# Kernel tuning notes

Hardware: AMD Instinct MI355X
Metric: run time of the kernel (lower is better)

Reference implementation:

```python
import jax, jax.numpy as jnp
import numpy as np

HEADS = 16
NUM_CHUNKS = 8  # min(int(log2(4096))+1, 8)


def setup_inputs() -> dict:
    key = jax.random.key(0)
    ks = jax.random.split(key, 6)
    B, T, C = 4, 4096, 1024
    s = 1.0 / np.sqrt(C)
    x = jax.random.normal(ks[0], (B, T, C), jnp.float32)
    Wqkv = jax.random.normal(ks[1], (3 * C, C), jnp.float32) * s
    Wout = jax.random.normal(ks[2], (C, C), jnp.float32) * s
    bout = jnp.zeros((C,), jnp.float32)
    Wl1 = jax.random.normal(ks[3], (64, 1), jnp.float32)
    bl1 = jnp.zeros((64,), jnp.float32)
    Wl2 = jax.random.normal(ks[4], (HEADS, 64), jnp.float32) * 0.125
    bl2 = jnp.zeros((HEADS,), jnp.float32)
    return dict(x=x, Wqkv=Wqkv, Wout=Wout, bout=bout, Wl1=Wl1, bl1=bl1, Wl2=Wl2, bl2=bl2)


def reference(x, Wqkv, Wout, bout, Wl1, bl1, Wl2, bl2):
    B, T, C = x.shape
    H = HEADS
    dh = C // H
    nc = NUM_CHUNKS
    cs = T // nc
    scale = dh ** (-0.5)

    # qkv projection (torch Linear: x @ W.T), split, to [B,H,T,dh]
    qkv = x @ Wqkv.T  # [B,T,3C]
    q, k, v = jnp.split(qkv, 3, axis=-1)
    def heads(t):
        return t.reshape(B, T, H, dh).transpose(0, 2, 1, 3)
    q, k, v = heads(q), heads(k), heads(v)

    # lambda gates from log positions: [T,1] -> [T,H] -> [H,T]
    log_pos = jnp.log(jnp.arange(T, dtype=jnp.float32) + 1.0)[:, None]
    h1 = jax.nn.relu(log_pos @ Wl1.T + bl1)            # [T,64]
    lam = jax.nn.sigmoid(h1 @ Wl2.T + bl2).T           # [H,T]
    lam = lam.reshape(H, nc, cs)                        # per-chunk key gates

    # block-local (chunked) attention, fully vectorized over chunks
    qc = q.reshape(B, H, nc, cs, dh)
    kc = k.reshape(B, H, nc, cs, dh)
    vc = v.reshape(B, H, nc, cs, dh)
    scores = jnp.einsum('bhnqd,bhnkd->bhnqk', qc, kc) * scale
    scores = scores * lam[None, :, :, None, :]          # gate keys pre-softmax
    attn = jax.nn.softmax(scores, axis=-1)
    out = jnp.einsum('bhnqk,bhnkd->bhnqd', attn, vc)    # [B,H,nc,cs,dh]

    out = out.reshape(B, H, T, dh).transpose(0, 2, 1, 3).reshape(B, T, C)
    return out @ Wout.T + bout
```

## Files before the change

### kernel.cpp

```cpp
#include <hip/hip_runtime.h>
#include <hip/hip_bf16.h>

typedef unsigned short u16;
typedef __attribute__((ext_vector_type(8))) short v8s;
typedef __attribute__((ext_vector_type(4))) float v4f;
typedef __attribute__((ext_vector_type(4))) unsigned v4u;

#define DEV __device__ __forceinline__

DEV u16 f2bf(float f) {
  union { float f; unsigned u; } v; v.f = f;
  unsigned r = v.u + 0x7fffu + ((v.u >> 16) & 1u);
  return (u16)(r >> 16);
}

DEV unsigned pk2bf(float a, float b) {
  float2 t; t.x = a; t.y = b;
  __hip_bfloat162 p = __float22bfloat162_rn(t);
  union { __hip_bfloat162 h; unsigned u; } c; c.h = p;
  return c.u;
}

DEV void gload_lds16(const void* g, void* l) {
  __builtin_amdgcn_global_load_lds(
      (const __attribute__((address_space(1))) void*)g,
      (__attribute__((address_space(3))) void*)l, 16, 0, 0);
}

__global__ __launch_bounds__(256) void cvt_bf16(const float* __restrict__ in,
                                                u16* __restrict__ out, int n4) {
  int i = blockIdx.x * 256 + threadIdx.x;
  if (i >= n4) return;
  float4 v = ((const float4*)in)[i];
  ushort4 o;
  o.x = f2bf(v.x); o.y = f2bf(v.y); o.z = f2bf(v.z); o.w = f2bf(v.w);
  ((ushort4*)out)[i] = o;
}

__global__ __launch_bounds__(256) void lam_kernel(const float* __restrict__ Wl1,
    const float* __restrict__ bl1, const float* __restrict__ Wl2,
    const float* __restrict__ bl2, float* __restrict__ lam) {
  int t = blockIdx.x * 256 + threadIdx.x;
  float lp = logf((float)t + 1.0f);
  float h1[64];
#pragma unroll
  for (int j = 0; j < 64; ++j) h1[j] = fmaxf(lp * Wl1[j] + bl1[j], 0.0f);
#pragma unroll 1
  for (int h = 0; h < 16; ++h) {
    float z = bl2[h];
#pragma unroll
    for (int j = 0; j < 64; ++j) z += h1[j] * Wl2[h * 64 + j];
    lam[h * 4096 + t] = 0.125f / (1.0f + expf(-z));
  }
}

template <int MH, int NH>
DEV void mfma16(v4f (&acc)[8][4], const v8s (&a)[4][2], const v8s (&b)[2][2]) {
#pragma unroll
  for (int kk = 0; kk < 2; ++kk)
#pragma unroll
    for (int i = 0; i < 4; ++i)
#pragma unroll
      for (int j = 0; j < 2; ++j)
        acc[MH * 4 + i][NH * 2 + j] = __builtin_amdgcn_mfma_f32_16x16x32_bf16(
            a[i][kk], b[j][kk], acc[MH * 4 + i][NH * 2 + j], 0, 0, 0);
}

DEV void ldA(v8s (&a)[4][2], const u16* Ab, int wr, int mh, int lane) {
  const int l15 = lane & 15, g = lane >> 4;
#pragma unroll
  for (int i = 0; i < 4; ++i) {
    const int row = wr * 128 + mh * 64 + i * 16 + l15;
#pragma unroll
    for (int kk = 0; kk < 2; ++kk)
      a[i][kk] = *(const v8s*)(Ab + row * 64 + (((kk * 4 + g) ^ (row & 7)) << 3));
  }
}

DEV void ldB(v8s (&b)[2][2], const u16* Bb, int wc, int nh, int lane) {
  const int l15 = lane & 15, g = lane >> 4;
#pragma unroll
  for (int j = 0; j < 2; ++j) {
    const int row = nh * 128 + wc * 32 + j * 16 + l15;
#pragma unroll
    for (int kk = 0; kk < 2; ++kk)
      b[j][kk] = *(const v8s*)(Bb + row * 64 + (((kk * 4 + g) ^ (row & 7)) << 3));
  }
}

template <int OUTF32>
__global__ __launch_bounds__(512, 2) void gemm256(const u16* __restrict__ A,
    const u16* __restrict__ Bt, void* __restrict__ Cout,
    const float* __restrict__ bias, int M, int N, int K) {
  __shared__ u16 As[2][256 * 64];
  __shared__ u16 Bs[2][256 * 64];
  const int tid = threadIdx.x;
  const int lane = tid & 63;
  const int nbn = N >> 8;
  const int nwg = gridDim.x;
  int wg = blockIdx.x;
  wg = (wg & 7) * (nwg >> 3) + (wg >> 3);
  const int m0 = (wg / nbn) << 8;
  const int n0 = (wg % nbn) << 8;
  const int wid = tid >> 6;
  const int wr = wid >> 2;
  const int wc = wid & 3;
  const int nkt = K >> 6;
  const int nit = nkt >> 1;

  auto SAu = [&](int buf, int kt, int u) {
    const int ur = tid >> 3;
    const int slot = (tid & 7) ^ (ur & 7);
    gload_lds16(A + (size_t)(m0 + u * 64 + ur) * K + kt * 64 + slot * 8,
                &As[buf][u * 4096 + (tid & ~63) * 8]);
  };
  auto SBu = [&](int buf, int kt, int u) {
    const int q = tid >> 3;
    const int grow = (((u & 1) * 2 + (q >> 5)) << 6) + ((u >> 1) << 5) + (q & 31);
    const int slot = (tid & 7) ^ (q & 7);
    gload_lds16(Bt + (size_t)(n0 + grow) * K + kt * 64 + slot * 8,
                &Bs[buf][u * 4096 + (tid & ~63) * 8]);
  };
  auto SA_ = [&](int buf, int kt, int mh) { SAu(buf, kt, mh); SAu(buf, kt, 2 + mh); };
  auto SB_ = [&](int buf, int kt, int nh) { SBu(buf, kt, nh * 2); SBu(buf, kt, nh * 2 + 1); };

  v4f acc[8][4] = {};
  v8s a[4][2], b[2][2];

  SA_(0, 0, 0); SB_(0, 0, 0); SB_(0, 0, 1); SA_(0, 0, 1);
  SA_(1, 1 < nkt ? 1 : 0, 0); SB_(1, 1 < nkt ? 1 : 0, 1); SA_(1, 1 < nkt ? 1 : 0, 1);
  asm volatile("s_waitcnt vmcnt(6)" ::: "memory");
  asm volatile("s_barrier" ::: "memory");

#define PHASE(MHc, NHc, STAGE, VM)                      \
  STAGE;                                                \
  asm volatile("s_barrier" ::: "memory");               \
  __builtin_amdgcn_sched_barrier(0);                    \
  __builtin_amdgcn_s_setprio(1);                        \
  mfma16<MHc, NHc>(acc, a, b);                          \
  __builtin_amdgcn_s_setprio(0);                        \
  if (VM) asm volatile("s_waitcnt vmcnt(6)" ::: "memory"); \
  asm volatile("s_barrier" ::: "memory");

  for (int it = 0; it < nit; ++it) {
    const int t0 = 2 * it;
    const int tn = t0 + 1;
    const int ta = (t0 + 2 < nkt) ? t0 + 2 : nkt - 1;
    const int tb = (t0 + 3 < nkt) ? t0 + 3 : nkt - 1;
    ldA(a, As[0], wr, 0, lane); ldB(b, Bs[0], wc, 0, lane);
    PHASE(0, 0, SB_(1, tn, 0), 0);
    ldB(b, Bs[0], wc, 1, lane);
    PHASE(0, 1, SA_(0, ta, 0), 0);
    ldA(a, As[0], wr, 1, lane);
    PHASE(1, 1, SB_(0, ta, 1), 0);
    ldB(b, Bs[0], wc, 0, lane);
    PHASE(1, 0, SA_(0, ta, 1), 1);
    ldA(a, As[1], wr, 0, lane); ldB(b, Bs[1], wc, 0, lane);
    PHASE(0, 0, SB_(0, ta, 0), 0);
    ldB(b, Bs[1], wc, 1, lane);
    PHASE(0, 1, SA_(1, tb, 0), 0);
    ldA(a, As[1], wr, 1, lane);
    PHASE(1, 1, SB_(1, tb, 1), 0);
    ldB(b, Bs[1], wc, 0, lane);
    PHASE(1, 0, SA_(1, tb, 1), 1);
  }
#undef PHASE

  const int l15 = lane & 15, g4 = (lane >> 4) * 4;
#pragma unroll
  for (int i = 0; i < 8; ++i) {
#pragma unroll
    for (int j = 0; j < 4; ++j) {
      const int gr = m0 + wr * 128 + i * 16 + g4;
      const int gc = n0 + wc * 64 + j * 16 + l15;
      float bv = OUTF32 ? bias[gc] : 0.0f;
#pragma unroll
      for (int r = 0; r < 4; ++r) {
        float val = acc[i][j][r];
        if (OUTF32) ((float*)Cout)[(size_t)(gr + r) * N + gc] = val + bv;
        else ((u16*)Cout)[(size_t)(gr + r) * N + gc] = f2bf(val);
      }
    }
  }
}

__global__ __launch_bounds__(512, 2) void attn_chunk(const u16* __restrict__ qkv,
    const float* __restrict__ lam, u16* __restrict__ aout) {
  __shared__ u16 Ksm[512 * 64];
  __shared__ u16 Vt[64 * 520];
  __shared__ float lam_s[512];

  const int tid = threadIdx.x;
  const int lane = tid & 63;
  const int wid = tid >> 6;
  const int blk = blockIdx.x;
  const int c = blk & 7;
  const int h = (blk >> 3) & 15;
  const int b = blk >> 7;
  const size_t tok0 = (size_t)b * 4096 + c * 512;
  const u16* qb = qkv + tok0 * 3072 + h * 64;
  const u16* kb = qb + 1024;
  const u16* vb = qb + 2048;

  lam_s[tid] = lam[h * 4096 + c * 512 + tid];

#pragma unroll
  for (int i = 0; i < 8; ++i) {
    const int r = i * 64 + wid * 8 + (lane >> 3);
    const int f = (r & 3) | (((r >> 3) & 1) << 2);
    gload_lds16(kb + (size_t)r * 3072 + (((lane & 7) ^ f) << 3),
                &Ksm[(i * 64 + wid * 8) * 64]);
  }
  {
    const int pr = tid & 255;
    const int db0 = (tid >> 8) * 4;
#pragma unroll
    for (int dbi = 0; dbi < 4; ++dbi) {
      const int d0 = (db0 + dbi) * 8;
      v8s v0 = *(const v8s*)(vb + (size_t)(2 * pr) * 3072 + d0);
      v8s v1 = *(const v8s*)(vb + (size_t)(2 * pr + 1) * 3072 + d0);
#pragma unroll
      for (int j = 0; j < 8; ++j) {
        unsigned pk = (unsigned)(u16)v0[j] | ((unsigned)(u16)v1[j] << 16);
        *(unsigned*)&Vt[(d0 + j) * 520 + 2 * pr] = pk;
      }
    }
  }
  __syncthreads();

  const int l15 = lane & 15;
  const int gg = lane >> 4;
  const int rbase = ((l15 >> 2) << 3) + (l15 & 3);
  const int fsl = (l15 & 3) | (((l15 >> 2) & 1) << 2);
  const int sl0 = ((gg ^ fsl) << 3);
  const int sl1 = (((4 + gg) ^ fsl) << 3);

#pragma unroll 1
  for (int pass = 0; pass < 4; ++pass) {
    const int q0 = pass * 128 + wid * 16;
    const v8s qf0 = *(const v8s*)(qb + (size_t)(q0 + l15) * 3072 + gg * 8);
    const v8s qf1 = *(const v8s*)(qb + (size_t)(q0 + l15) * 3072 + 32 + gg * 8);

    float m = -1e30f, sum = 0.0f;
    v4f o[4] = {};

#pragma unroll 1
    for (int qtr = 0; qtr < 4; ++qtr) {
      v4f s[8];
#pragma unroll
      for (int kpl = 0; kpl < 4; ++kpl) {
#pragma unroll
        for (int hh = 0; hh < 2; ++hh) {
          const int rw = (qtr * 128 + kpl * 32 + rbase + hh * 4) << 6;
          v4f z = {0.f, 0.f, 0.f, 0.f};
          z = __builtin_amdgcn_mfma_f32_16x16x32_bf16(
              *(const v8s*)&Ksm[rw + sl0], qf0, z, 0, 0, 0);
          z = __builtin_amdgcn_mfma_f32_16x16x32_bf16(
              *(const v8s*)&Ksm[rw + sl1], qf1, z, 0, 0, 0);
          const v4f lv = *(const v4f*)&lam_s[qtr * 128 + kpl * 32 + gg * 8 + hh * 4];
          s[kpl * 2 + hh] = z * lv;
        }
      }
      v4f vm = s[0];
#pragma unroll
      for (int kt = 1; kt < 8; ++kt)
#pragma unroll
        for (int r = 0; r < 4; ++r) vm[r] = fmaxf(vm[r], s[kt][r]);
      float qmax = fmaxf(fmaxf(vm[0], vm[1]), fmaxf(vm[2], vm[3]));
      qmax = fmaxf(qmax, __shfl_xor(qmax, 16));
      qmax = fmaxf(qmax, __shfl_xor(qmax, 32));
      const float newm = fmaxf(m, qmax);
      const float scale = __expf(m - newm);
      m = newm;
      float psum = 0.f;
#pragma unroll
      for (int kt = 0; kt < 8; ++kt)
#pragma unroll
        for (int r = 0; r < 4; ++r) {
          s[kt][r] = __expf(s[kt][r] - m);
          psum += s[kt][r];
        }
      sum = sum * scale + psum;
#pragma unroll
      for (int dt = 0; dt < 4; ++dt)
#pragma unroll
        for (int r = 0; r < 4; ++r) o[dt][r] *= scale;

#pragma unroll
      for (int kpl = 0; kpl < 4; ++kpl) {
        v4u pwv;
        pwv.x = pk2bf(s[2 * kpl][0], s[2 * kpl][1]);
        pwv.y = pk2bf(s[2 * kpl][2], s[2 * kpl][3]);
        pwv.z = pk2bf(s[2 * kpl + 1][0], s[2 * kpl + 1][1]);
        pwv.w = pk2bf(s[2 * kpl + 1][2], s[2 * kpl + 1][3]);
        const v8s pf = __builtin_bit_cast(v8s, pwv);
#pragma unroll
        for (int dt = 0; dt < 4; ++dt) {
          const v8s vf = *(const v8s*)&Vt[(dt * 16 + l15) * 520 +
                                          (qtr * 4 + kpl) * 32 + gg * 8];
          o[dt] = __builtin_amdgcn_mfma_f32_16x16x32_bf16(vf, pf, o[dt], 0, 0, 0);
        }
      }
    }

    sum += __shfl_xor(sum, 16);
    sum += __shfl_xor(sum, 32);
    const float sminv = 1.0f / sum;

    const size_t obase = (tok0 + q0 + l15) * 1024 + h * 64;
#pragma unroll
    for (int dt = 0; dt < 4; ++dt) {
      ushort4 w;
      w.x = f2bf(o[dt][0] * sminv); w.y = f2bf(o[dt][1] * sminv);
      w.z = f2bf(o[dt][2] * sminv); w.w = f2bf(o[dt][3] * sminv);
      *(ushort4*)&aout[obase + dt * 16 + gg * 4] = w;
    }
  }
}

extern "C" void kernel_launch(void* const* d_in, const int* in_sizes, int n_in,
                              void* d_out, int out_size, void* d_ws, size_t ws_size,
                              hipStream_t stream) {
  const float* x    = (const float*)d_in[0];
  const float* Wqkv = (const float*)d_in[1];
  const float* Wout = (const float*)d_in[2];
  const float* bout = (const float*)d_in[3];
  const float* Wl1  = (const float*)d_in[4];
  const float* bl1  = (const float*)d_in[5];
  const float* Wl2  = (const float*)d_in[6];
  const float* bl2  = (const float*)d_in[7];
  float* out = (float*)d_out;

  char* ws = (char*)d_ws;
  u16* xbf    = (u16*)ws; ws += (size_t)16384 * 1024 * 2;
  u16* wqkvbf = (u16*)ws; ws += (size_t)3072 * 1024 * 2;
  u16* woutbf = (u16*)ws; ws += (size_t)1024 * 1024 * 2;
  u16* qkvbf  = (u16*)ws; ws += (size_t)16384 * 3072 * 2;
  u16* aoutbf = (u16*)ws; ws += (size_t)16384 * 1024 * 2;
  float* lam  = (float*)ws; ws += (size_t)16 * 4096 * 4;

  cvt_bf16<<<16384, 256, 0, stream>>>(x, xbf, 16777216 / 4);
  cvt_bf16<<<3072, 256, 0, stream>>>(Wqkv, wqkvbf, 3145728 / 4);
  cvt_bf16<<<1024, 256, 0, stream>>>(Wout, woutbf, 1048576 / 4);
  lam_kernel<<<16, 256, 0, stream>>>(Wl1, bl1, Wl2, bl2, lam);

  gemm256<0><<<dim3((16384 / 256) * (3072 / 256)), 512, 0, stream>>>(
      xbf, wqkvbf, qkvbf, nullptr, 16384, 3072, 1024);

  attn_chunk<<<512, 512, 0, stream>>>(qkvbf, lam, aoutbf);

  gemm256<1><<<dim3((16384 / 256) * (1024 / 256)), 512, 0, stream>>>(
      aoutbf, woutbf, out, bout, 16384, 1024, 1024);
}
```

Baseline: 278.0 us.

## Restructure GEMM main loop into four wider MFMA phases with full B fragment

Each warp now loads the whole B fragment (4x2) at once and runs 32 MFMAs per phase instead of 16. That halves the barrier-separated phases per K-iteration from eight to four. The global-to-LDS staging schedule is reorganized to match. This reduces barrier and LDS-read overhead per MFMA, at the cost of more registers for B fragments and a different, riskier prefetch/waitcnt ordering.

```diff
diff --git a/kernel.cpp b/kernel.cpp
--- a/kernel.cpp
+++ b/kernel.cpp
@@ -54,16 +54,16 @@
   }
 }
 
-template <int MH, int NH>
-DEV void mfma16(v4f (&acc)[8][4], const v8s (&a)[4][2], const v8s (&b)[2][2]) {
+template <int MH>
+DEV void mfma32(v4f (&acc)[8][4], const v8s (&a)[4][2], const v8s (&b)[4][2]) {
 #pragma unroll
   for (int kk = 0; kk < 2; ++kk)
 #pragma unroll
     for (int i = 0; i < 4; ++i)
 #pragma unroll
-      for (int j = 0; j < 2; ++j)
-        acc[MH * 4 + i][NH * 2 + j] = __builtin_amdgcn_mfma_f32_16x16x32_bf16(
-            a[i][kk], b[j][kk], acc[MH * 4 + i][NH * 2 + j], 0, 0, 0);
+      for (int j = 0; j < 4; ++j)
+        acc[MH * 4 + i][j] = __builtin_amdgcn_mfma_f32_16x16x32_bf16(
+            a[i][kk], b[j][kk], acc[MH * 4 + i][j], 0, 0, 0);
 }
 
 DEV void ldA(v8s (&a)[4][2], const u16* Ab, int wr, int mh, int lane) {
@@ -77,11 +77,11 @@
   }
 }
 
-DEV void ldB(v8s (&b)[2][2], const u16* Bb, int wc, int nh, int lane) {
+DEV void ldB4(v8s (&b)[4][2], const u16* Bb, int wc, int lane) {
   const int l15 = lane & 15, g = lane >> 4;
 #pragma unroll
-  for (int j = 0; j < 2; ++j) {
-    const int row = nh * 128 + wc * 32 + j * 16 + l15;
+  for (int j = 0; j < 4; ++j) {
+    const int row = (j >> 1) * 128 + wc * 32 + (j & 1) * 16 + l15;
 #pragma unroll
     for (int kk = 0; kk < 2; ++kk)
       b[j][kk] = *(const v8s*)(Bb + row * 64 + (((kk * 4 + g) ^ (row & 7)) << 3));
@@ -125,44 +125,36 @@
   auto SB_ = [&](int buf, int kt, int nh) { SBu(buf, kt, nh * 2); SBu(buf, kt, nh * 2 + 1); };
 
   v4f acc[8][4] = {};
-  v8s a[4][2], b[2][2];
-
-  SA_(0, 0, 0); SB_(0, 0, 0); SB_(0, 0, 1); SA_(0, 0, 1);
-  SA_(1, 1 < nkt ? 1 : 0, 0); SB_(1, 1 < nkt ? 1 : 0, 1); SA_(1, 1 < nkt ? 1 : 0, 1);
+  v8s a[4][2], b[4][2];
+
+  SA_(0, 0, 0); SA_(0, 0, 1); SB_(0, 0, 0); SB_(0, 0, 1);
+  SA_(1, 1, 0); SB_(1, 1, 0); SB_(1, 1, 1);
   asm volatile("s_waitcnt vmcnt(6)" ::: "memory");
   asm volatile("s_barrier" ::: "memory");
 
-#define PHASE(MHc, NHc, STAGE, VM)                      \
-  STAGE;                                                \
-  asm volatile("s_barrier" ::: "memory");               \
-  __builtin_amdgcn_sched_barrier(0);                    \
-  __builtin_amdgcn_s_setprio(1);                        \
-  mfma16<MHc, NHc>(acc, a, b);                          \
-  __builtin_amdgcn_s_setprio(0);                        \
-  if (VM) asm volatile("s_waitcnt vmcnt(6)" ::: "memory"); \
+#define PHASE(MHc, VM, ...)                                 \
+  do { __VA_ARGS__; } while (0);                            \
+  asm volatile("s_barrier" ::: "memory");                   \
+  __builtin_amdgcn_sched_barrier(0);                        \
+  __builtin_amdgcn_s_setprio(1);                            \
+  mfma32<MHc>(acc, a, b);                                   \
+  __builtin_amdgcn_s_setprio(0);                            \
+  if (VM) asm volatile("s_waitcnt vmcnt(6)" ::: "memory");  \
   asm volatile("s_barrier" ::: "memory");
 
   for (int it = 0; it < nit; ++it) {
     const int t0 = 2 * it;
-    const int tn = t0 + 1;
-    const int ta = (t0 + 2 < nkt) ? t0 + 2 : nkt - 1;
-    const int tb = (t0 + 3 < nkt) ? t0 + 3 : nkt - 1;
-    ldA(a, As[0], wr, 0, lane); ldB(b, Bs[0], wc, 0, lane);
-    PHASE(0, 0, SB_(1, tn, 0), 0);
-    ldB(b, Bs[0], wc, 1, lane);
-    PHASE(0, 1, SA_(0, ta, 0), 0);
+    const int t1 = t0 + 1;
+    const int t2 = (t0 + 2 < nkt) ? t0 + 2 : nkt - 1;
+    const int t3 = (t0 + 3 < nkt) ? t0 + 3 : nkt - 1;
+    ldA(a, As[0], wr, 0, lane); ldB4(b, Bs[0], wc, lane);
+    PHASE(0, 0, SAu(1, t1, 1); SAu(1, t1, 3));
     ldA(a, As[0], wr, 1, lane);
-    PHASE(1, 1, SB_(0, ta, 1), 0);
-    ldB(b, Bs[0], wc, 0, lane);
-    PHASE(1, 0, SA_(0, ta, 1), 1);
-    ldA(a, As[1], wr, 0, lane); ldB(b, Bs[1], wc, 0, lane);
-    PHASE(0, 0, SB_(0, ta, 0), 0);
-    ldB(b, Bs[1], wc, 1, lane);
-    PHASE(0, 1, SA_(1, tb, 0), 0);
+    PHASE(1, 1, SB_(0, t2, 0); SB_(0, t2, 1); SAu(0, t2, 0); SAu(0, t2, 2));
+    ldA(a, As[1], wr, 0, lane); ldB4(b, Bs[1], wc, lane);
+    PHASE(0, 0, SAu(0, t2, 1); SAu(0, t2, 3));
     ldA(a, As[1], wr, 1, lane);
-    PHASE(1, 1, SB_(1, tb, 1), 0);
-    ldB(b, Bs[1], wc, 0, lane);
-    PHASE(1, 0, SA_(1, tb, 1), 1);
+    PHASE(1, 1, SB_(1, t3, 0); SB_(1, t3, 1); SAu(1, t3, 0); SAu(1, t3, 2));
   }
 #undef PHASE
 
```

New measurement: 264.6 us. -4.8%, faster.
